# Kernel optimization log

Hardware: AMD Instinct MI355X
Metric: run time of the kernel (lower is better)

## Reference

```python
import jax, jax.numpy as jnp
import numpy as np

N = 100000
MUL = 16


def _build_cg():
    # Real-basis Clebsch-Gordan (Wigner-3j-style) coefficients, shape (2l1+1, 2l2+1, 2lo+1),
    # each normalized to unit Frobenius norm per output component (e3nn component normalization).
    eps = np.zeros((3, 3, 3), np.float32)
    for a, b, c in [(0, 1, 2), (1, 2, 0), (2, 0, 1)]:
        eps[a, b, c] = 1.0
        eps[a, c, b] = -1.0
    s2 = np.float32(1.0 / np.sqrt(2.0))
    q = np.zeros((5, 3, 3), np.float32)  # l=2 real harmonics: xy, yz, 3z^2-r^2, xz, x^2-y^2
    q[0, 0, 1] = q[0, 1, 0] = s2
    q[1, 1, 2] = q[1, 2, 1] = s2
    q[2] = np.diag([-1.0, -1.0, 2.0]).astype(np.float32) / np.sqrt(6.0)
    q[3, 0, 2] = q[3, 2, 0] = s2
    q[4] = np.diag([1.0, -1.0, 0.0]).astype(np.float32) * s2
    cg000 = jnp.ones((1, 1, 1), jnp.float32)                                   # 0e x 0e -> 0e
    cg011 = jnp.asarray(np.eye(3, dtype=np.float32)[None])                      # 0e x 1o -> 1o
    cg110 = jnp.asarray((np.eye(3, dtype=np.float32) / np.sqrt(3.0))[:, :, None])  # 1o x 1o -> 0e
    cg111 = jnp.asarray(eps * s2)                                               # 1o x 1o -> 1e
    cg112 = jnp.asarray(np.transpose(q, (1, 2, 0)))                             # 1o x 1o -> 2e
    return cg000, cg011, cg110, cg111, cg112


def _path(x1, x2, cg, w, alpha):
    # 'uvw' tensor-product path: out[z,w,m] = alpha * sum_{u,v,i,j} x1[z,u,i] x2[z,v,j] cg[i,j,m] w[u,v,w]
    # Contraction order chosen to keep the largest intermediate at [z,u,w,j].
    t = jnp.einsum('zvj,uvw->zuwj', x2, w)
    s = jnp.einsum('zui,zuwj->zwij', x1, t)
    return alpha * jnp.einsum('zwij,ijm->zwm', s, cg)


def _tensor_square(x, w0, w1, w2, w3, w4):
    n = x.shape[0]
    x0 = x[:, :MUL].reshape(n, MUL, 1)       # 16x0e
    x1 = x[:, MUL:].reshape(n, MUL, 3)       # 16x1o
    cg000, cg011, cg110, cg111, cg112 = _build_cg()
    a2 = 1.0 / np.sqrt(MUL * MUL * 2.0)      # 0e output receives 2 paths
    a1 = 1.0 / np.sqrt(MUL * MUL * 1.0)
    o_0e = _path(x0, x0, cg000, w0, a2) + _path(x1, x1, cg110, w2, a2)
    o_1o = _path(x0, x1, cg011, w1, a1)
    o_1e = _path(x1, x1, cg111, w3, a1)
    o_2e = _path(x1, x1, cg112, w4, a1)
    return jnp.concatenate([o.reshape(n, -1) for o in (o_0e, o_1o, o_1e, o_2e)], axis=1)


def setup_inputs() -> dict:
    key = jax.random.key(0)
    kx, k0, k1, k2, k3, k4 = jax.random.split(key, 6)
    return {
        'x': jax.random.normal(kx, (N, MUL * 1 + MUL * 3), jnp.float32),
        'w0': jax.random.normal(k0, (MUL, MUL, MUL), jnp.float32),
        'w1': jax.random.normal(k1, (MUL, MUL, MUL), jnp.float32),
        'w2': jax.random.normal(k2, (MUL, MUL, MUL), jnp.float32),
        'w3': jax.random.normal(k3, (MUL, MUL, MUL), jnp.float32),
        'w4': jax.random.normal(k4, (MUL, MUL, MUL), jnp.float32),
    }


def reference(x, w0, w1, w2, w3, w4):
    return _tensor_square(x, w0, w1, w2, w3, w4)
```

## Files before the change

kernel.cpp:

```cpp
#include <hip/hip_runtime.h>
#include <hip/hip_bf16.h>

typedef __attribute__((ext_vector_type(8))) short short8;
typedef __attribute__((ext_vector_type(4))) float float4v;
typedef __attribute__((ext_vector_type(2))) float float2v;

#define S_A 0.04419417382415922f
#define S_B 0.025515518153991442f
#define S_C 0.0625f

static __device__ __forceinline__ unsigned pkbf(float a, float b) {
#if __has_builtin(__builtin_amdgcn_cvt_pk_bf16_f32)
    auto v = __builtin_amdgcn_cvt_pk_bf16_f32(a, b);
    return __builtin_bit_cast(unsigned, v);
#else
    unsigned ua = __builtin_bit_cast(unsigned, a);
    unsigned ub = __builtin_bit_cast(unsigned, b);
    ua += 0x7fffu + ((ua >> 16) & 1u);
    ub += 0x7fffu + ((ub >> 16) & 1u);
    return __builtin_amdgcn_perm(ub, ua, 0x07060302);
#endif
}

__global__ void wprep_kernel(const float* __restrict__ wA, const float* __restrict__ wB,
                             const float* __restrict__ wC, const float* __restrict__ wD,
                             const float* __restrict__ wE, unsigned short* __restrict__ wout)
{
    int e = blockIdx.x * 256 + threadIdx.x;
    if (e >= 5 * 4096) return;
    int p = e >> 12;
    int rem = e & 4095;
    const float* wp = (p == 0) ? wA : (p == 1) ? wB : (p == 2) ? wC : (p == 3) ? wD : wE;
    unsigned u = __builtin_bit_cast(unsigned, wp[rem]);
    u += 0x7fffu + ((u >> 16) & 1u);
    int k = rem >> 4, w = rem & 15;
    int c = k >> 5, kk = k & 31;
    int lane = ((kk >> 3) << 4) | w;
    int j = kk & 7;
    wout[(((c * 5 + p) * 64 + lane) << 3) | j] = (unsigned short)(u >> 16);
}

__global__ __launch_bounds__(256, 2)
void tsq_kernel(const float* __restrict__ x,
                const unsigned short* __restrict__ wfrag,
                float* __restrict__ out,
                int nrows)
{
    __shared__ __attribute__((aligned(16))) float xlds[64 * 68];

    const int tid = threadIdx.x;

    {
        const long long rowbase = (long long)blockIdx.x * 64;
        const float* xg = x + rowbase * 64;
        #pragma unroll
        for (int q = 0; q < 4; q++) {
            int f = q * 1024 + tid * 4;
            int row = f >> 6, col = f & 63;
            float4v v = {0.f, 0.f, 0.f, 0.f};
            if (rowbase + row < nrows) v = *(const float4v*)(xg + f);
            *(float4v*)&xlds[row * 68 + col] = v;
        }
    }
    __syncthreads();

    const int wave = tid >> 6;
    const int l = tid & 63;
    const long long z0 = (long long)blockIdx.x * 64 + wave * 16;
    if (z0 >= nrows) return;

    const int r  = l & 15;
    const int g  = l >> 4;
    const int v0 = (g & 1) * 8;
    const int uo = g >> 1;
    const float* xr = &xlds[(wave * 16 + r) * 68];

    float2v A0v[4], Xv[4], Yv[4], Zv[4];
    {
        float a[8], b[24];
        #pragma unroll
        for (int q = 0; q < 2; q++) *(float4v*)&a[q * 4] = *(const float4v*)(xr + v0 + q * 4);
        #pragma unroll
        for (int q = 0; q < 6; q++) *(float4v*)&b[q * 4] = *(const float4v*)(xr + 16 + v0 * 3 + q * 4);
        #pragma unroll
        for (int t = 0; t < 4; t++) {
            A0v[t] = (float2v){a[2 * t], a[2 * t + 1]};
            Xv[t]  = (float2v){b[6 * t + 0], b[6 * t + 3]};
            Yv[t]  = (float2v){b[6 * t + 1], b[6 * t + 4]};
            Zv[t]  = (float2v){b[6 * t + 2], b[6 * t + 5]};
        }
    }

    float4v acc[13];
    #pragma unroll
    for (int m = 0; m < 13; m++) acc[m] = (float4v){0.f, 0.f, 0.f, 0.f};

    constexpr int pm[13] = {0, 1, 2, 2, 2, 3, 3, 3, 4, 4, 4, 4, 4};

    const short8* wbase = (const short8*)wfrag;

    #pragma unroll
    for (int c = 0; c < 8; c++) {
        short8 wf[5];
        #pragma unroll
        for (int p = 0; p < 5; p++) wf[p] = wbase[(c * 5 + p) * 64 + l];

        const int u = c * 2 + uo;
        const float u0 = xr[u];
        const float ux = xr[16 + u * 3 + 0];
        const float uy = xr[16 + u * 3 + 1];
        const float uz = xr[16 + u * 3 + 2];

        unsigned fri[13][4];
        #pragma unroll
        for (int t = 0; t < 4; t++) {
            const float2v X = Xv[t], Y = Yv[t], Z = Zv[t];
            const float2v p00 = ux * X, p01 = ux * Y, p02 = ux * Z;
            const float2v p10 = uy * X, p11 = uy * Y, p12 = uy * Z;
            const float2v p20 = uz * X, p21 = uz * Y, p22 = uz * Z;
            float2v bv[13];
            bv[0]  = u0 * A0v[t];
            bv[1]  = p00 + p11 + p22;
            bv[2]  = u0 * X;
            bv[3]  = u0 * Y;
            bv[4]  = u0 * Z;
            bv[5]  = p12 - p21;
            bv[6]  = p20 - p02;
            bv[7]  = p01 - p10;
            bv[8]  = p01 + p10;
            bv[9]  = p12 + p21;
            bv[10] = 2.0f * p22 - p00 - p11;
            bv[11] = p02 + p20;
            bv[12] = p00 - p11;
            #pragma unroll
            for (int m = 0; m < 13; m++) fri[m][t] = pkbf(bv[m].x, bv[m].y);
        }

        #pragma unroll
        for (int m = 0; m < 13; m++) {
            short8 frm = __builtin_bit_cast(short8, *(unsigned __attribute__((ext_vector_type(4)))*)fri[m]);
            acc[m] = __builtin_amdgcn_mfma_f32_16x16x32_bf16(frm, wf[pm[m]], acc[m], 0, 0, 0);
        }
    }

    const int w = r;
    float* outp = out + (z0 + g * 4) * 192;
    #pragma unroll
    for (int reg = 0; reg < 4; reg++) {
        float* rowp = outp + reg * 192;
        rowp[w] = S_A * acc[0][reg] + S_B * acc[1][reg];
        rowp[16 + w * 3 + 0]  = S_C * acc[2][reg];
        rowp[16 + w * 3 + 1]  = S_C * acc[3][reg];
        rowp[16 + w * 3 + 2]  = S_C * acc[4][reg];
        rowp[64 + w * 3 + 0]  = S_A * acc[5][reg];
        rowp[64 + w * 3 + 1]  = S_A * acc[6][reg];
        rowp[64 + w * 3 + 2]  = S_A * acc[7][reg];
        rowp[112 + w * 5 + 0] = S_A * acc[8][reg];
        rowp[112 + w * 5 + 1] = S_A * acc[9][reg];
        rowp[112 + w * 5 + 2] = S_B * acc[10][reg];
        rowp[112 + w * 5 + 3] = S_A * acc[11][reg];
        rowp[112 + w * 5 + 4] = S_A * acc[12][reg];
    }
}

extern "C" void kernel_launch(void* const* d_in, const int* in_sizes, int n_in,
                              void* d_out, int out_size, void* d_ws, size_t ws_size,
                              hipStream_t stream) {
    const float* x  = (const float*)d_in[0];
    const float* w0 = (const float*)d_in[1];
    const float* w1 = (const float*)d_in[2];
    const float* w2 = (const float*)d_in[3];
    const float* w3 = (const float*)d_in[4];
    const float* w4 = (const float*)d_in[5];
    float* out = (float*)d_out;
    unsigned short* wfrag = (unsigned short*)d_ws;
    (void)ws_size; (void)n_in; (void)out_size;

    const int nrows = in_sizes[0] / 64;
    const int nblocks = (nrows + 63) / 64;

    wprep_kernel<<<dim3(80), dim3(256), 0, stream>>>(w0, w2, w1, w3, w4, wfrag);
    tsq_kernel<<<dim3(nblocks), dim3(256), 0, stream>>>(x, wfrag, out, nrows);
}
```

Before: 139.6 us.

## Split output components across waves with smaller 16-row blocks

Restructures the tensor-square kernel so each block handles 16 rows, and each of its four waves computes a distinct subset of output irreps (1o, 0e/2e-diag, 1e, 2e-offdiag). Each wave issues only a few MFMAs per chunk and holds far fewer accumulators, reducing register pressure and raising occupancy. In exchange, x-derived products are partially recomputed across waves, the block count quadruples, and wave workloads are slightly unbalanced.

```diff
diff --git a/kernel.cpp b/kernel.cpp
--- a/kernel.cpp
+++ b/kernel.cpp
@@ -4,6 +4,7 @@
 typedef __attribute__((ext_vector_type(8))) short short8;
 typedef __attribute__((ext_vector_type(4))) float float4v;
 typedef __attribute__((ext_vector_type(2))) float float2v;
+typedef __attribute__((ext_vector_type(4))) unsigned uint4v;
 
 #define S_A 0.04419417382415922f
 #define S_B 0.025515518153991442f
@@ -40,127 +41,171 @@
     wout[(((c * 5 + p) * 64 + lane) << 3) | j] = (unsigned short)(u >> 16);
 }
 
-__global__ __launch_bounds__(256, 2)
+template<int G>
+static __device__ __forceinline__ void run_group(
+    const float* __restrict__ xr, int l, const short8* __restrict__ wbase,
+    float* __restrict__ out, long long z0)
+{
+    const int r  = l & 15;
+    const int g  = l >> 4;
+    const int v0 = (g & 1) * 8;
+    const int uo = g >> 1;
+
+    float2v Xv[4], Yv[4], Zv[4];
+    float2v A0v[4];
+    {
+        float b[24];
+        #pragma unroll
+        for (int q = 0; q < 6; q++)
+            *(float4v*)&b[q * 4] = *(const float4v*)(xr + 16 + v0 * 3 + q * 4);
+        #pragma unroll
+        for (int t = 0; t < 4; t++) {
+            Xv[t] = (float2v){b[6 * t + 0], b[6 * t + 3]};
+            Yv[t] = (float2v){b[6 * t + 1], b[6 * t + 4]};
+            Zv[t] = (float2v){b[6 * t + 2], b[6 * t + 5]};
+        }
+        if constexpr (G == 1) {
+            float a[8];
+            #pragma unroll
+            for (int q = 0; q < 2; q++)
+                *(float4v*)&a[q * 4] = *(const float4v*)(xr + v0 + q * 4);
+            #pragma unroll
+            for (int t = 0; t < 4; t++) A0v[t] = (float2v){a[2 * t], a[2 * t + 1]};
+        }
+    }
+
+    constexpr int NS = (G == 1) ? 4 : 3;
+    float4v acc[NS];
+    #pragma unroll
+    for (int s = 0; s < NS; s++) acc[s] = (float4v){0.f, 0.f, 0.f, 0.f};
+
+    #pragma unroll
+    for (int c = 0; c < 8; c++) {
+        short8 wfA, wfB, wfC;
+        if constexpr (G == 0) wfA = wbase[(c * 5 + 2) * 64 + l];
+        if constexpr (G == 1) {
+            wfA = wbase[(c * 5 + 0) * 64 + l];
+            wfB = wbase[(c * 5 + 1) * 64 + l];
+            wfC = wbase[(c * 5 + 4) * 64 + l];
+        }
+        if constexpr (G == 2) wfA = wbase[(c * 5 + 3) * 64 + l];
+        if constexpr (G == 3) wfA = wbase[(c * 5 + 4) * 64 + l];
+
+        const int u = c * 2 + uo;
+        float u0 = 0.f, ux = 0.f, uy = 0.f, uz = 0.f;
+        if constexpr (G == 0 || G == 1) u0 = xr[u];
+        if constexpr (G != 0) {
+            ux = xr[16 + u * 3 + 0];
+            uy = xr[16 + u * 3 + 1];
+            uz = xr[16 + u * 3 + 2];
+        }
+
+        unsigned fri[NS][4];
+        #pragma unroll
+        for (int t = 0; t < 4; t++) {
+            const float2v X = Xv[t], Y = Yv[t], Z = Zv[t];
+            if constexpr (G == 0) {
+                float2v b2 = u0 * X, b3 = u0 * Y, b4 = u0 * Z;
+                fri[0][t] = pkbf(b2.x, b2.y);
+                fri[1][t] = pkbf(b3.x, b3.y);
+                fri[2][t] = pkbf(b4.x, b4.y);
+            }
+            if constexpr (G == 1) {
+                float2v p00 = ux * X, p11 = uy * Y, p22 = uz * Z;
+                float2v b0 = u0 * A0v[t];
+                float2v b1 = p00 + p11 + p22;
+                float2v b10 = 2.0f * p22 - p00 - p11;
+                float2v b12 = p00 - p11;
+                fri[0][t] = pkbf(b0.x, b0.y);
+                fri[1][t] = pkbf(b1.x, b1.y);
+                fri[2][t] = pkbf(b10.x, b10.y);
+                fri[3][t] = pkbf(b12.x, b12.y);
+            }
+            if constexpr (G == 2) {
+                float2v p01 = ux * Y, p02 = ux * Z, p10 = uy * X;
+                float2v p12 = uy * Z, p20 = uz * X, p21 = uz * Y;
+                float2v b5 = p12 - p21, b6 = p20 - p02, b7 = p01 - p10;
+                fri[0][t] = pkbf(b5.x, b5.y);
+                fri[1][t] = pkbf(b6.x, b6.y);
+                fri[2][t] = pkbf(b7.x, b7.y);
+            }
+            if constexpr (G == 3) {
+                float2v p01 = ux * Y, p02 = ux * Z, p10 = uy * X;
+                float2v p12 = uy * Z, p20 = uz * X, p21 = uz * Y;
+                float2v b8 = p01 + p10, b9 = p12 + p21, b11 = p02 + p20;
+                fri[0][t] = pkbf(b8.x, b8.y);
+                fri[1][t] = pkbf(b9.x, b9.y);
+                fri[2][t] = pkbf(b11.x, b11.y);
+            }
+        }
+
+        #pragma unroll
+        for (int s = 0; s < NS; s++) {
+            short8 frm = __builtin_bit_cast(short8, *(uint4v*)fri[s]);
+            const short8& wf = (G == 1) ? ((s == 0) ? wfA : (s == 1) ? wfB : wfC) : wfA;
+            acc[s] = __builtin_amdgcn_mfma_f32_16x16x32_bf16(frm, wf, acc[s], 0, 0, 0);
+        }
+    }
+
+    const int w = r;
+    float* outp = out + (z0 + g * 4) * 192;
+    #pragma unroll
+    for (int reg = 0; reg < 4; reg++) {
+        float* rowp = outp + reg * 192;
+        if constexpr (G == 0) {
+            rowp[16 + w * 3 + 0] = S_C * acc[0][reg];
+            rowp[16 + w * 3 + 1] = S_C * acc[1][reg];
+            rowp[16 + w * 3 + 2] = S_C * acc[2][reg];
+        }
+        if constexpr (G == 1) {
+            rowp[w]               = S_A * acc[0][reg] + S_B * acc[1][reg];
+            rowp[112 + w * 5 + 2] = S_B * acc[2][reg];
+            rowp[112 + w * 5 + 4] = S_A * acc[3][reg];
+        }
+        if constexpr (G == 2) {
+            rowp[64 + w * 3 + 0] = S_A * acc[0][reg];
+            rowp[64 + w * 3 + 1] = S_A * acc[1][reg];
+            rowp[64 + w * 3 + 2] = S_A * acc[2][reg];
+        }
+        if constexpr (G == 3) {
+            rowp[112 + w * 5 + 0] = S_A * acc[0][reg];
+            rowp[112 + w * 5 + 1] = S_A * acc[1][reg];
+            rowp[112 + w * 5 + 3] = S_A * acc[2][reg];
+        }
+    }
+}
+
+__global__ __launch_bounds__(256)
 void tsq_kernel(const float* __restrict__ x,
                 const unsigned short* __restrict__ wfrag,
                 float* __restrict__ out,
                 int nrows)
 {
-    __shared__ __attribute__((aligned(16))) float xlds[64 * 68];
+    __shared__ __attribute__((aligned(16))) float xlds[16 * 68];
 
     const int tid = threadIdx.x;
+    const long long z0 = (long long)blockIdx.x * 16;
 
     {
-        const long long rowbase = (long long)blockIdx.x * 64;
-        const float* xg = x + rowbase * 64;
-        #pragma unroll
-        for (int q = 0; q < 4; q++) {
-            int f = q * 1024 + tid * 4;
-            int row = f >> 6, col = f & 63;
-            float4v v = {0.f, 0.f, 0.f, 0.f};
-            if (rowbase + row < nrows) v = *(const float4v*)(xg + f);
-            *(float4v*)&xlds[row * 68 + col] = v;
-        }
+        const float* xg = x + z0 * 64;
+        int f = tid * 4;
+        int row = f >> 6, col = f & 63;
+        float4v v = {0.f, 0.f, 0.f, 0.f};
+        if (z0 + row < nrows) v = *(const float4v*)(xg + f);
+        *(float4v*)&xlds[row * 68 + col] = v;
     }
     __syncthreads();
+    if (z0 >= nrows) return;
 
     const int wave = tid >> 6;
     const int l = tid & 63;
-    const long long z0 = (long long)blockIdx.x * 64 + wave * 16;
-    if (z0 >= nrows) return;
-
-    const int r  = l & 15;
-    const int g  = l >> 4;
-    const int v0 = (g & 1) * 8;
-    const int uo = g >> 1;
-    const float* xr = &xlds[(wave * 16 + r) * 68];
-
-    float2v A0v[4], Xv[4], Yv[4], Zv[4];
-    {
-        float a[8], b[24];
-        #pragma unroll
-        for (int q = 0; q < 2; q++) *(float4v*)&a[q * 4] = *(const float4v*)(xr + v0 + q * 4);
-        #pragma unroll
-        for (int q = 0; q < 6; q++) *(float4v*)&b[q * 4] = *(const float4v*)(xr + 16 + v0 * 3 + q * 4);
-        #pragma unroll
-        for (int t = 0; t < 4; t++) {
-            A0v[t] = (float2v){a[2 * t], a[2 * t + 1]};
-            Xv[t]  = (float2v){b[6 * t + 0], b[6 * t + 3]};
-            Yv[t]  = (float2v){b[6 * t + 1], b[6 * t + 4]};
-            Zv[t]  = (float2v){b[6 * t + 2], b[6 * t + 5]};
-        }
-    }
-
-    float4v acc[13];
-    #pragma unroll
-    for (int m = 0; m < 13; m++) acc[m] = (float4v){0.f, 0.f, 0.f, 0.f};
-
-    constexpr int pm[13] = {0, 1, 2, 2, 2, 3, 3, 3, 4, 4, 4, 4, 4};
-
+    const float* xr = &xlds[(l & 15) * 68];
     const short8* wbase = (const short8*)wfrag;
 
-    #pragma unroll
-    for (int c = 0; c < 8; c++) {
-        short8 wf[5];
-        #pragma unroll
-        for (int p = 0; p < 5; p++) wf[p] = wbase[(c * 5 + p) * 64 + l];
-
-        const int u = c * 2 + uo;
-        const float u0 = xr[u];
-        const float ux = xr[16 + u * 3 + 0];
-        const float uy = xr[16 + u * 3 + 1];
-        const float uz = xr[16 + u * 3 + 2];
-
-        unsigned fri[13][4];
-        #pragma unroll
-        for (int t = 0; t < 4; t++) {
-            const float2v X = Xv[t], Y = Yv[t], Z = Zv[t];
-            const float2v p00 = ux * X, p01 = ux * Y, p02 = ux * Z;
-            const float2v p10 = uy * X, p11 = uy * Y, p12 = uy * Z;
-            const float2v p20 = uz * X, p21 = uz * Y, p22 = uz * Z;
-            float2v bv[13];
-            bv[0]  = u0 * A0v[t];
-            bv[1]  = p00 + p11 + p22;
-            bv[2]  = u0 * X;
-            bv[3]  = u0 * Y;
-            bv[4]  = u0 * Z;
-            bv[5]  = p12 - p21;
-            bv[6]  = p20 - p02;
-            bv[7]  = p01 - p10;
-            bv[8]  = p01 + p10;
-            bv[9]  = p12 + p21;
-            bv[10] = 2.0f * p22 - p00 - p11;
-            bv[11] = p02 + p20;
-            bv[12] = p00 - p11;
-            #pragma unroll
-            for (int m = 0; m < 13; m++) fri[m][t] = pkbf(bv[m].x, bv[m].y);
-        }
-
-        #pragma unroll
-        for (int m = 0; m < 13; m++) {
-            short8 frm = __builtin_bit_cast(short8, *(unsigned __attribute__((ext_vector_type(4)))*)fri[m]);
-            acc[m] = __builtin_amdgcn_mfma_f32_16x16x32_bf16(frm, wf[pm[m]], acc[m], 0, 0, 0);
-        }
-    }
-
-    const int w = r;
-    float* outp = out + (z0 + g * 4) * 192;
-    #pragma unroll
-    for (int reg = 0; reg < 4; reg++) {
-        float* rowp = outp + reg * 192;
-        rowp[w] = S_A * acc[0][reg] + S_B * acc[1][reg];
-        rowp[16 + w * 3 + 0]  = S_C * acc[2][reg];
-        rowp[16 + w * 3 + 1]  = S_C * acc[3][reg];
-        rowp[16 + w * 3 + 2]  = S_C * acc[4][reg];
-        rowp[64 + w * 3 + 0]  = S_A * acc[5][reg];
-        rowp[64 + w * 3 + 1]  = S_A * acc[6][reg];
-        rowp[64 + w * 3 + 2]  = S_A * acc[7][reg];
-        rowp[112 + w * 5 + 0] = S_A * acc[8][reg];
-        rowp[112 + w * 5 + 1] = S_A * acc[9][reg];
-        rowp[112 + w * 5 + 2] = S_B * acc[10][reg];
-        rowp[112 + w * 5 + 3] = S_A * acc[11][reg];
-        rowp[112 + w * 5 + 4] = S_A * acc[12][reg];
-    }
+    if      (wave == 0) run_group<0>(xr, l, wbase, out, z0);
+    else if (wave == 1) run_group<1>(xr, l, wbase, out, z0);
+    else if (wave == 2) run_group<2>(xr, l, wbase, out, z0);
+    else                run_group<3>(xr, l, wbase, out, z0);
 }
 
 extern "C" void kernel_launch(void* const* d_in, const int* in_sizes, int n_in,
@@ -177,7 +222,7 @@
     (void)ws_size; (void)n_in; (void)out_size;
 
     const int nrows = in_sizes[0] / 64;
-    const int nblocks = (nrows + 63) / 64;
+    const int nblocks = (nrows + 15) / 16;
 
     wprep_kernel<<<dim3(80), dim3(256), 0, stream>>>(w0, w2, w1, w3, w4, wfrag);
     tsq_kernel<<<dim3(nblocks), dim3(256), 0, stream>>>(x, wfrag, out, nrows);
```

Result: no change. 137.4 us (-1.6%).
